# Kernel optimization log

Hardware: AMD Instinct MI355X
Metric: run time of the kernel (lower is better)

## Reference

```python
import jax, jax.numpy as jnp
import numpy as np

B, L, C_IN = 8, 1024, 12
D_MODEL, D_STATE, D_CONV, D_INNER, DT_RANK = 128, 16, 4, 256, 8
H, HD = 4, 32
LSTM_H, FC_H, NCLS = 128, 128, 5


def setup_inputs():
    ks = jax.random.split(jax.random.key(0), 16)

    def rn(k, shape, s=0.02):
        return jax.random.normal(k, shape, dtype=jnp.float32) * s

    return {
        "x": jax.random.normal(ks[0], (B, L, C_IN), dtype=jnp.float32),
        "mamba_proj_w": rn(ks[1], (C_IN, D_MODEL)),
        "mamba_proj_b": jnp.zeros((D_MODEL,), jnp.float32),
        "in_proj_w": rn(ks[2], (D_MODEL, 2 * D_INNER)),
        "conv_w": rn(ks[3], (D_INNER, D_CONV), 0.2),
        "conv_b": jnp.zeros((D_INNER,), jnp.float32),
        "x_proj_w": rn(ks[4], (D_INNER, DT_RANK + 2 * D_STATE)),
        "dt_proj_w": rn(ks[5], (DT_RANK, D_INNER), 0.1),
        "dt_proj_b": jnp.full((D_INNER,), -4.6, jnp.float32),
        "A_log": jnp.log(jnp.broadcast_to(jnp.arange(1, D_STATE + 1, dtype=jnp.float32), (D_INNER, D_STATE))),
        "Dp": jnp.ones((D_INNER,), jnp.float32),
        "out_proj_w": rn(ks[6], (D_INNER, D_MODEL)),
        "lstm_w_ih": rn(ks[7], (C_IN, 4 * LSTM_H), 0.05),
        "lstm_w_hh": rn(ks[8], (LSTM_H, 4 * LSTM_H), 0.05),
        "lstm_b": jnp.zeros((4 * LSTM_H,), jnp.float32),
        "ca_w": rn(ks[9], (2, 4, D_MODEL, D_MODEL)),
        "ca_b": jnp.zeros((2, 4, D_MODEL), jnp.float32),
        "ln_g": jnp.ones((2, D_MODEL), jnp.float32),
        "ln_b": jnp.zeros((2, D_MODEL), jnp.float32),
        "fc1_w": rn(ks[10], (2 * D_MODEL, FC_H)),
        "fc1_b": jnp.zeros((FC_H,), jnp.float32),
        "fc2_w": rn(ks[11], (FC_H, NCLS)),
        "fc2_b": jnp.zeros((NCLS,), jnp.float32),
    }


def _ln(x, g, b):
    m = jnp.mean(x, -1, keepdims=True)
    v = jnp.var(x, -1, keepdims=True)
    return (x - m) * jax.lax.rsqrt(v + 1e-5) * g + b


def _cross_attn(q_in, kv_in, w, b):
    # w: (4, d_model, d_model) q,k,v,out; b: (4, d_model)
    bsz, lq, lk = q_in.shape[0], q_in.shape[1], kv_in.shape[1]
    Q = (q_in @ w[0] + b[0]).reshape(bsz, lq, H, HD).transpose(0, 2, 1, 3)
    K = (kv_in @ w[1] + b[1]).reshape(bsz, lk, H, HD).transpose(0, 2, 1, 3)
    V = (kv_in @ w[2] + b[2]).reshape(bsz, lk, H, HD).transpose(0, 2, 1, 3)
    s = jnp.einsum('bhqd,bhkd->bhqk', Q, K) / float(np.sqrt(HD))
    a = jax.nn.softmax(s, axis=-1)
    o = jnp.einsum('bhqk,bhkd->bhqd', a, V).transpose(0, 2, 1, 3).reshape(bsz, lq, H * HD)
    return o @ w[3] + b[3]


def _mamba(u, in_proj_w, conv_w, conv_b, x_proj_w, dt_proj_w, dt_proj_b, A_log, Dp, out_proj_w):
    # u: (B, L, d_model) -> (B, L, d_model); standard Mamba selective-scan block
    xz = u @ in_proj_w  # (B, L, 2*d_inner)
    xm, z = jnp.split(xz, 2, axis=-1)
    # causal depthwise conv1d (kernel d_conv, left-padded)
    xp = jnp.pad(xm, ((0, 0), (D_CONV - 1, 0), (0, 0)))
    xc = sum(xp[:, k:k + xm.shape[1], :] * conv_w[:, k] for k in range(D_CONV)) + conv_b
    xc = jax.nn.silu(xc)  # (B, L, d_inner)
    dbl = xc @ x_proj_w
    dt = dbl[..., :DT_RANK]
    Bm = dbl[..., DT_RANK:DT_RANK + D_STATE]
    Cm = dbl[..., DT_RANK + D_STATE:]
    delta = jax.nn.softplus(dt @ dt_proj_w + dt_proj_b)  # (B, L, d_inner)
    A = -jnp.exp(A_log)  # (d_inner, d_state)
    dA = jnp.exp(delta[..., None] * A)                          # (B, L, d_inner, d_state)
    dBu = delta[..., None] * Bm[:, :, None, :] * xc[..., None]  # (B, L, d_inner, d_state)

    def step(h, inp):
        dA_t, dBu_t = inp
        h = dA_t * h + dBu_t
        return h, h

    h0 = jnp.zeros((xc.shape[0], D_INNER, D_STATE), xc.dtype)
    _, hs = jax.lax.scan(step, h0, (dA.swapaxes(0, 1), dBu.swapaxes(0, 1)))  # hs: (L, B, d_inner, d_state)
    y = jnp.einsum('lbds,bls->bld', hs, Cm) + Dp * xc
    y = y * jax.nn.silu(z)
    return y @ out_proj_w


def _forward(x, mamba_proj_w, mamba_proj_b, in_proj_w, conv_w, conv_b, x_proj_w, dt_proj_w, dt_proj_b, A_log, Dp, out_proj_w, lstm_w_ih, lstm_w_hh, lstm_b, ca_w, ca_b, ln_g, ln_b, fc1_w, fc1_b, fc2_w, fc2_b):
    H_M = _mamba(x @ mamba_proj_w + mamba_proj_b, in_proj_w, conv_w, conv_b, x_proj_w, dt_proj_w, dt_proj_b, A_log, Dp, out_proj_w)

    def lstm_step(carry, x_t):
        h, c = carry
        g = x_t @ lstm_w_ih + h @ lstm_w_hh + lstm_b
        i, f, gg, o = jnp.split(g, 4, axis=-1)  # torch gate order i,f,g,o
        c = jax.nn.sigmoid(f) * c + jax.nn.sigmoid(i) * jnp.tanh(gg)
        h = jax.nn.sigmoid(o) * jnp.tanh(c)
        return (h, c), h

    h0 = jnp.zeros((x.shape[0], LSTM_H), x.dtype)
    _, hs = jax.lax.scan(lstm_step, (h0, h0), x.swapaxes(0, 1))
    H_L = hs.swapaxes(0, 1)  # lstm_proj is Identity (lstm_hidden == d_model)

    H_Lu = _ln(H_L + _cross_attn(H_L, H_M, ca_w[0], ca_b[0]), ln_g[0], ln_b[0])
    H_Mu = _ln(H_M + _cross_attn(H_M, H_L, ca_w[1], ca_b[1]), ln_g[1], ln_b[1])
    fused = jnp.concatenate([H_Mu.mean(1), H_Lu.mean(1)], axis=1)  # (B, 2*d_model)
    return jax.nn.relu(fused @ fc1_w + fc1_b) @ fc2_w + fc2_b


def reference(x, mamba_proj_w, mamba_proj_b, in_proj_w, conv_w, conv_b, x_proj_w, dt_proj_w, dt_proj_b, A_log, Dp, out_proj_w, lstm_w_ih, lstm_w_hh, lstm_b, ca_w, ca_b, ln_g, ln_b, fc1_w, fc1_b, fc2_w, fc2_b):
    return _forward(x, mamba_proj_w, mamba_proj_b, in_proj_w, conv_w, conv_b, x_proj_w, dt_proj_w, dt_proj_b, A_log, Dp, out_proj_w, lstm_w_ih, lstm_w_hh, lstm_b, ca_w, ca_b, ln_g, ln_b, fc1_w, fc1_b, fc2_w, fc2_b)
```

## Files before the change

### kernel.cpp

```cpp
#include <hip/hip_runtime.h>
#include <hip/hip_bf16.h>
#include <math.h>

#define B_     8
#define L_     1024
#define BL_    8192
#define C_IN_  12
#define DM_    128
#define DS_    16
#define DC_    4
#define DI_    256
#define DTR_   8
#define NH_    4
#define HD_    32
#define LH_    128
#define FCH_   128
#define NCLS_  5

#define OFF_U      0u
#define OFF_XC     1048576u
#define OFF_DBL    3145728u
#define OFF_DELTA  3670016u
#define OFF_YG     5767168u
#define OFF_XZ     7864320u
#define OFF_XG     12058624u
#define OFF_HM     12058624u
#define OFF_HL     0u
#define OFF_PL     1048576u
#define OFF_PM     4194304u
#define OFF_AO0    7340032u
#define OFF_AO1    8388608u
#define OFF_T0     9437184u
#define OFF_T1     10485760u
#define OFF_WPK    14155776u
#define OFF_HLU    14286848u
#define OFF_HMU    15335424u
#define OFF_POOL   16384000u

static __device__ __forceinline__ float fexpf_(float x){ return __builtin_amdgcn_exp2f(x*1.44269504089f); }
static __device__ __forceinline__ float fsig(float x){ return __builtin_amdgcn_rcpf(1.f + fexpf_(-x)); }
static __device__ __forceinline__ float ftanh(float x){ return 1.f - 2.f*__builtin_amdgcn_rcpf(1.f + fexpf_(2.f*x)); }
static __device__ __forceinline__ float siluf(float x){ return x*fsig(x); }
static __device__ __forceinline__ float softplusf(float x){
  return (x > 0.f) ? x + log1pf(expf(-x)) : log1pf(expf(x));
}
static __device__ __forceinline__ float qbcast_xor1(float x){
  return __int_as_float(__builtin_amdgcn_mov_dpp(__float_as_int(x), 0xB1, 0xF, 0xF, true));
}
static __device__ __forceinline__ float qbcast_xor2(float x){
  return __int_as_float(__builtin_amdgcn_mov_dpp(__float_as_int(x), 0x4E, 0xF, 0xF, true));
}

__global__ __launch_bounds__(256) void gemm_kernel(
    const float* __restrict__ A, int lda,
    const float* __restrict__ W,
    const float* __restrict__ bias,
    float* __restrict__ C,
    int M, int N, int K, int act)
{
  __shared__ float As[64][17];
  __shared__ float Ws[16][65];
  const int tid = threadIdx.x;
  const int tx = tid & 15, ty = tid >> 4;
  const int m0 = blockIdx.y * 64, n0 = blockIdx.x * 64;
  float acc[4][4];
  #pragma unroll
  for (int i=0;i<4;i++)
    #pragma unroll
    for (int j=0;j<4;j++) acc[i][j]=0.f;

  for (int k0=0;k0<K;k0+=16){
    const int ar = tid >> 2, ac4 = (tid & 3) * 4;
    #pragma unroll
    for (int j=0;j<4;j++){
      int kk = k0 + ac4 + j;
      As[ar][ac4+j] = (kk < K) ? A[(size_t)(m0+ar)*lda + kk] : 0.f;
    }
    const int wc = tid & 63, wr0 = (tid >> 6) * 4;
    #pragma unroll
    for (int j=0;j<4;j++){
      int kk = k0 + wr0 + j;
      Ws[wr0+j][wc] = (kk < K && (n0+wc) < N) ? W[(size_t)kk*N + n0 + wc] : 0.f;
    }
    __syncthreads();
    #pragma unroll
    for (int kk=0;kk<16;kk++){
      float a[4], w[4];
      #pragma unroll
      for (int i=0;i<4;i++) a[i] = As[ty*4+i][kk];
      #pragma unroll
      for (int j=0;j<4;j++) w[j] = Ws[kk][tx*4+j];
      #pragma unroll
      for (int i=0;i<4;i++)
        #pragma unroll
        for (int j=0;j<4;j++)
          acc[i][j] = fmaf(a[i], w[j], acc[i][j]);
    }
    __syncthreads();
  }
  #pragma unroll
  for (int i=0;i<4;i++){
    int m = m0 + ty*4 + i;
    #pragma unroll
    for (int j=0;j<4;j++){
      int n = n0 + tx*4 + j;
      if (n < N){
        float v = acc[i][j] + (bias ? bias[n] : 0.f);
        if (act == 1) v = softplusf(v);
        C[(size_t)m*N + n] = v;
      }
    }
  }
}

__global__ __launch_bounds__(256,2) void gemm128_kernel(
    const float* __restrict__ A, int lda,
    const float* __restrict__ W,
    const float* __restrict__ bias,
    float* __restrict__ C,
    int M, int N, int K, int act)
{
  __shared__ float As[8][132];
  __shared__ float Ws[8][132];
  const int tid = threadIdx.x;
  const int tx = tid & 15, ty = tid >> 4;
  const int m0 = blockIdx.y * 128, n0 = blockIdx.x * 128;
  const int ar = tid >> 1, akq = (tid & 1) * 4;
  const int wkr = tid >> 5, wnc = (tid & 31) * 4;
  float acc[8][8];
  #pragma unroll
  for (int i=0;i<8;i++)
    #pragma unroll
    for (int j=0;j<8;j++) acc[i][j]=0.f;

  for (int k0=0;k0<K;k0+=8){
    float4 av = *(const float4*)&A[(size_t)(m0+ar)*lda + k0 + akq];
    float4 wv = *(const float4*)&W[(size_t)(k0+wkr)*N + n0 + wnc];
    __syncthreads();
    As[akq+0][ar]=av.x; As[akq+1][ar]=av.y; As[akq+2][ar]=av.z; As[akq+3][ar]=av.w;
    *(float4*)&Ws[wkr][wnc] = wv;
    __syncthreads();
    #pragma unroll
    for (int kk=0;kk<8;kk++){
      float4 a0 = *(const float4*)&As[kk][ty*8];
      float4 a1 = *(const float4*)&As[kk][ty*8+4];
      float4 w0 = *(const float4*)&Ws[kk][tx*8];
      float4 w1 = *(const float4*)&Ws[kk][tx*8+4];
      float a[8] = {a0.x,a0.y,a0.z,a0.w,a1.x,a1.y,a1.z,a1.w};
      float w[8] = {w0.x,w0.y,w0.z,w0.w,w1.x,w1.y,w1.z,w1.w};
      #pragma unroll
      for (int i=0;i<8;i++)
        #pragma unroll
        for (int j=0;j<8;j++)
          acc[i][j] = fmaf(a[i], w[j], acc[i][j]);
    }
  }
  #pragma unroll
  for (int i=0;i<8;i++){
    int m = m0 + ty*8 + i;
    #pragma unroll
    for (int j=0;j<8;j++){
      int n = n0 + tx*8 + j;
      float v = acc[i][j] + (bias ? bias[n] : 0.f);
      if (act == 1) v = softplusf(v);
      C[(size_t)m*N + n] = v;
    }
  }
}

__global__ __launch_bounds__(256) void conv_silu_kernel(
    const float* __restrict__ xz, const float* __restrict__ conv_w,
    const float* __restrict__ conv_b, float* __restrict__ xc)
{
  int idx = blockIdx.x * 256 + threadIdx.x;
  if (idx >= BL_*DI_) return;
  int d = idx & (DI_-1);
  int bl = idx >> 8;
  int l = bl & (L_-1), b = bl >> 10;
  float acc = conv_b[d];
  #pragma unroll
  for (int k=0;k<DC_;k++){
    int lk = l - (DC_-1) + k;
    if (lk >= 0)
      acc = fmaf(xz[((size_t)((b<<10)|lk))*512 + d], conv_w[d*DC_+k], acc);
  }
  xc[idx] = siluf(acc);
}

__global__ __launch_bounds__(512,2) void scan_lstm_kernel(
    const float* __restrict__ delta, const float* __restrict__ dbl,
    const float* __restrict__ xc, const float* __restrict__ xz,
    const float* __restrict__ A_log, const float* __restrict__ Dp,
    float* __restrict__ yg,
    const float* __restrict__ xg, const float* __restrict__ w_hh,
    float* __restrict__ HL)
{
  __shared__ float sd[32][32], sx[32][32], sz[32][32];
  __shared__ float sB[32][17], sC[32][17];
  __shared__ float lh[2][128];
  const int tid = threadIdx.x;

  if (blockIdx.x < 64){
    const int b = blockIdx.x >> 3;
    const int d0 = (blockIdx.x & 7) * 32;
    const int dl = tid >> 4, s = tid & 15;
    const float A = -expf(A_log[(d0+dl)*DS_ + s]);
    const float Dv = Dp[d0+dl];
    float h = 0.f;
    const size_t base = (size_t)b * L_;
    for (int t0=0; t0<L_; t0+=32){
      __syncthreads();
      #pragma unroll
      for (int i0=0;i0<2;i0++){
        int i = tid + i0*512;
        int tl = i >> 5, e = i & 31;
        size_t r = base + t0 + tl;
        sd[tl][e] = delta[r*256 + d0 + e];
        sx[tl][e] = xc[r*256 + d0 + e];
        sz[tl][e] = xz[r*512 + 256 + d0 + e];
      }
      {
        int tl = tid >> 4, e = tid & 15;
        size_t r = base + t0 + tl;
        sB[tl][e] = dbl[r*40 + DTR_ + e];
        sC[tl][e] = dbl[r*40 + DTR_ + DS_ + e];
      }
      __syncthreads();
      for (int j=0;j<32;j++){
        float dlt = sd[j][dl], xcv = sx[j][dl];
        float Bv = sB[j][s], Cv = sC[j][s];
        h = fmaf(fexpf_(dlt*A), h, (dlt*Bv)*xcv);
        float pr = h * Cv;
        pr += qbcast_xor1(pr);
        pr += qbcast_xor2(pr);
        pr += __shfl_xor(pr, 4);
        pr += __shfl_xor(pr, 8);
        if (s == 0){
          float y = pr + Dv * xcv;
          yg[(base + t0 + j)*256 + d0 + dl] = y * siluf(sz[j][dl]);
        }
      }
    }
  } else {
    const int b = blockIdx.x - 64;
    const int g = tid >> 2, p = tid & 3;
    float wi[32], wf[32], wg_[32], wo[32];
    #pragma unroll
    for (int jj=0;jj<8;jj++){
      const int j = (jj + 2*p) & 7;
      const float* wr = w_hh + (size_t)(32*p + 4*j)*512 + g;
      #pragma unroll
      for (int c=0;c<4;c++){
        wi [4*jj+c] = wr[(size_t)c*512];
        wf [4*jj+c] = wr[(size_t)c*512 + 128];
        wg_[4*jj+c] = wr[(size_t)c*512 + 256];
        wo [4*jj+c] = wr[(size_t)c*512 + 384];
      }
    }
    #pragma unroll
    for (int i=0;i<32;i++)
      asm volatile("" : "+v"(wi[i]), "+v"(wf[i]), "+v"(wg_[i]), "+v"(wo[i]));
    if (tid < 128) lh[0][tid] = 0.f;
    float creg = 0.f;
    const float* xgb = xg + (size_t)b * L_ * 512;
    float* HLb = HL + (size_t)b * L_ * 128;
    float xv0 = xgb[g], xv1 = xgb[128+g], xv2 = xgb[256+g], xv3 = xgb[384+g];
    __syncthreads();
    int cur = 0;
    for (int t=0;t<L_;t++){
      const float* hb = lh[cur] + 32*p;
      float a_i=0,a_f=0,a_g=0,a_o=0;
      #pragma unroll
      for (int jj=0;jj<8;jj++){
        const int j = (jj + 2*p) & 7;
        float4 hv = *(const float4*)(hb + 4*j);
        a_i = fmaf(hv.x, wi [4*jj+0], a_i);
        a_f = fmaf(hv.x, wf [4*jj+0], a_f);
        a_g = fmaf(hv.x, wg_[4*jj+0], a_g);
        a_o = fmaf(hv.x, wo [4*jj+0], a_o);
        a_i = fmaf(hv.y, wi [4*jj+1], a_i);
        a_f = fmaf(hv.y, wf [4*jj+1], a_f);
        a_g = fmaf(hv.y, wg_[4*jj+1], a_g);
        a_o = fmaf(hv.y, wo [4*jj+1], a_o);
        a_i = fmaf(hv.z, wi [4*jj+2], a_i);
        a_f = fmaf(hv.z, wf [4*jj+2], a_f);
        a_g = fmaf(hv.z, wg_[4*jj+2], a_g);
        a_o = fmaf(hv.z, wo [4*jj+2], a_o);
        a_i = fmaf(hv.w, wi [4*jj+3], a_i);
        a_f = fmaf(hv.w, wf [4*jj+3], a_f);
        a_g = fmaf(hv.w, wg_[4*jj+3], a_g);
        a_o = fmaf(hv.w, wo [4*jj+3], a_o);
      }
      float xn0=0.f,xn1=0.f,xn2=0.f,xn3=0.f;
      if (t+1 < L_){
        const float* xr = xgb + (size_t)(t+1)*512;
        xn0 = xr[g]; xn1 = xr[128+g]; xn2 = xr[256+g]; xn3 = xr[384+g];
      }
      a_i += qbcast_xor1(a_i); a_i += qbcast_xor2(a_i);
      a_f += qbcast_xor1(a_f); a_f += qbcast_xor2(a_f);
      a_g += qbcast_xor1(a_g); a_g += qbcast_xor2(a_g);
      a_o += qbcast_xor1(a_o); a_o += qbcast_xor2(a_o);
      float c = fsig(a_f + xv1)*creg + fsig(a_i + xv0)*ftanh(a_g + xv2);
      float hval = fsig(a_o + xv3)*ftanh(c);
      creg = c;
      if (p == 0){
        lh[cur^1][g] = hval;
        HLb[t*128 + g] = hval;
      }
      __syncthreads();
      cur ^= 1;
      xv0=xn0; xv1=xn1; xv2=xn2; xv3=xn3;
    }
  }
}

__global__ __launch_bounds__(256) void pack_kernel(
    const float* __restrict__ ca_w, const float* __restrict__ ca_b,
    float* __restrict__ wpk)
{
  int idx = blockIdx.x * 256 + threadIdx.x;
  if (idx >= 49152) return;
  int in = idx / 384, c = idx % 384;
  int seg = c >> 7, o = c & 127;
  int dL = (seg==0)?0:1;
  int iL = (seg==0)?0:((seg==1)?1:2);
  int dM = (seg==2)?1:0;
  int iM = (seg==0)?1:((seg==1)?2:0);
  wpk[idx]         = ca_w[(((size_t)(dL*4+iL))*128 + in)*128 + o];
  wpk[49152 + idx] = ca_w[(((size_t)(dM*4+iM))*128 + in)*128 + o];
  if (in == 0){
    wpk[98304 + c] = ca_b[(dL*4+iL)*128 + o];
    wpk[98688 + c] = ca_b[(dM*4+iM)*128 + o];
  }
}

__global__ __launch_bounds__(512,2) void attn_kernel(
    const float* __restrict__ PL, const float* __restrict__ PM,
    float* __restrict__ AO)
{
  __shared__ float Kt[2][32][32];
  __shared__ float Vt[2][32][32];
  __shared__ float po[256][33];
  __shared__ float pml[256][2];
  const int tid = threadIdx.x;
  const int q = tid & 255, half = tid >> 8;
  const int dir = blockIdx.z;
  const int bh = blockIdx.y;
  const int b = bh >> 2, hh = bh & 3;
  const int qg = blockIdx.x * 256 + q;
  const float* Qb; const float* Kb; const float* Vb;
  if (dir == 0){ Qb = PL;       Kb = PM;       Vb = PM + 128; }
  else         { Qb = PM + 256; Kb = PL + 128; Vb = PL + 256; }
  const size_t rowb = (size_t)b * L_;
  float qv[32];
  {
    const float4* qp = (const float4*)(Qb + (rowb + qg)*384 + hh*32);
    #pragma unroll
    for (int j=0;j<8;j++){
      float4 v = qp[j];
      qv[4*j]=v.x; qv[4*j+1]=v.y; qv[4*j+2]=v.z; qv[4*j+3]=v.w;
    }
  }
  #pragma unroll
  for (int i=0;i<32;i++) asm volatile("" : "+v"(qv[i]));
  float o[32];
  #pragma unroll
  for (int j=0;j<32;j++) o[j]=0.f;
  float m = -1e30f, l = 0.f;
  const float scale = 0.17677669529663687f;
  const int kbase = half * 512;
  for (int k0=0;k0<512;k0+=32){
    __syncthreads();
    #pragma unroll
    for (int i0=0;i0<4;i0++){
      int i = q + i0*256;
      int r = i >> 5, c = i & 31;
      Kt[half][r][c] = Kb[(rowb + kbase + k0 + r)*384 + hh*32 + c];
      Vt[half][r][c] = Vb[(rowb + kbase + k0 + r)*384 + hh*32 + c];
    }
    __syncthreads();
    for (int kk=0;kk<32;kk++){
      float d0=0.f,d1=0.f,d2=0.f,d3=0.f;
      #pragma unroll
      for (int j=0;j<32;j+=4){
        d0 = fmaf(qv[j],   Kt[half][kk][j],   d0);
        d1 = fmaf(qv[j+1], Kt[half][kk][j+1], d1);
        d2 = fmaf(qv[j+2], Kt[half][kk][j+2], d2);
        d3 = fmaf(qv[j+3], Kt[half][kk][j+3], d3);
      }
      float s4 = ((d0+d1)+(d2+d3))*scale;
      if (s4 > m + 8.f){
        float corr = fexpf_(m - s4);
        l *= corr;
        #pragma unroll
        for (int j=0;j<32;j++) o[j] *= corr;
        m = s4;
      }
      float p = fexpf_(s4 - m);
      l += p;
      #pragma unroll
      for (int j=0;j<32;j++) o[j] = fmaf(p, Vt[half][kk][j], o[j]);
    }
  }
  if (half == 1){
    pml[q][0] = m; pml[q][1] = l;
    #pragma unroll
    for (int j=0;j<32;j++) po[q][j] = o[j];
  }
  __syncthreads();
  if (half == 0){
    float m1 = pml[q][0], l1 = pml[q][1];
    float mm = fmaxf(m, m1);
    float c0 = fexpf_(m - mm), c1 = fexpf_(m1 - mm);
    float linv = 1.f / (l*c0 + l1*c1);
    float* op = AO + (size_t)dir*BL_*128 + (rowb + qg)*128 + hh*32;
    #pragma unroll
    for (int j=0;j<32;j+=4){
      float4 v;
      v.x = (o[j]*c0   + po[q][j]*c1)  *linv;
      v.y = (o[j+1]*c0 + po[q][j+1]*c1)*linv;
      v.z = (o[j+2]*c0 + po[q][j+2]*c1)*linv;
      v.w = (o[j+3]*c0 + po[q][j+3]*c1)*linv;
      *(float4*)(op + j) = v;
    }
  }
}

__global__ __launch_bounds__(64) void ln_kernel(
    const float* __restrict__ HL, const float* __restrict__ T0,
    const float* __restrict__ HM, const float* __restrict__ T1,
    const float* __restrict__ ln_g, const float* __restrict__ ln_b,
    float* __restrict__ HLu, float* __restrict__ HMu)
{
  const int row = blockIdx.x;
  const int which = blockIdx.y;
  const float* X = which ? HM : HL;
  const float* T = which ? T1 : T0;
  const float* g = ln_g + which*128;
  const float* bb = ln_b + which*128;
  float* O = which ? HMu : HLu;
  const int lane = threadIdx.x;
  float v0 = X[(size_t)row*128 + lane]      + T[(size_t)row*128 + lane];
  float v1 = X[(size_t)row*128 + 64 + lane] + T[(size_t)row*128 + 64 + lane];
  float s = v0 + v1, s2 = v0*v0 + v1*v1;
  #pragma unroll
  for (int off=1; off<64; off<<=1){ s += __shfl_xor(s,off); s2 += __shfl_xor(s2,off); }
  float mean = s * (1.f/128.f);
  float var = s2 * (1.f/128.f) - mean*mean;
  float r = rsqrtf(var + 1e-5f);
  O[(size_t)row*128 + lane]      = (v0 - mean)*r*g[lane]      + bb[lane];
  O[(size_t)row*128 + 64 + lane] = (v1 - mean)*r*g[64+lane]   + bb[64+lane];
}

__global__ __launch_bounds__(128) void pool_kernel(
    const float* __restrict__ HMu, const float* __restrict__ HLu,
    float* __restrict__ pooled)
{
  const int whichhalf = blockIdx.x;
  const int b = blockIdx.y;
  const int d = threadIdx.x;
  const float* S = whichhalf ? HLu : HMu;
  float s = 0.f;
  for (int t=0;t<L_;t++) s += S[((size_t)b*L_ + t)*128 + d];
  pooled[b*256 + whichhalf*128 + d] = s * (1.f/1024.f);
}

__global__ __launch_bounds__(128) void fc_kernel(
    const float* __restrict__ pooled,
    const float* __restrict__ fc1_w, const float* __restrict__ fc1_b,
    const float* __restrict__ fc2_w, const float* __restrict__ fc2_b,
    float* __restrict__ out)
{
  const int b = blockIdx.x;
  const int j = threadIdx.x;
  __shared__ float hid[128];
  float acc = fc1_b[j];
  for (int k=0;k<256;k++) acc = fmaf(pooled[b*256 + k], fc1_w[k*128 + j], acc);
  hid[j] = fmaxf(acc, 0.f);
  __syncthreads();
  if (j < NCLS_){
    float a = fc2_b[j];
    for (int k=0;k<128;k++) a = fmaf(hid[k], fc2_w[k*NCLS_ + j], a);
    out[b*NCLS_ + j] = a;
  }
}

extern "C" void kernel_launch(void* const* d_in, const int* in_sizes, int n_in,
                              void* d_out, int out_size, void* d_ws, size_t ws_size,
                              hipStream_t stream)
{
  const float* x            = (const float*)d_in[0];
  const float* mamba_proj_w = (const float*)d_in[1];
  const float* mamba_proj_b = (const float*)d_in[2];
  const float* in_proj_w    = (const float*)d_in[3];
  const float* conv_w       = (const float*)d_in[4];
  const float* conv_b       = (const float*)d_in[5];
  const float* x_proj_w     = (const float*)d_in[6];
  const float* dt_proj_w    = (const float*)d_in[7];
  const float* dt_proj_b    = (const float*)d_in[8];
  const float* A_log        = (const float*)d_in[9];
  const float* Dp           = (const float*)d_in[10];
  const float* out_proj_w   = (const float*)d_in[11];
  const float* lstm_w_ih    = (const float*)d_in[12];
  const float* lstm_w_hh    = (const float*)d_in[13];
  const float* lstm_b       = (const float*)d_in[14];
  const float* ca_w         = (const float*)d_in[15];
  const float* ca_b         = (const float*)d_in[16];
  const float* ln_g         = (const float*)d_in[17];
  const float* ln_b         = (const float*)d_in[18];
  const float* fc1_w        = (const float*)d_in[19];
  const float* fc1_b        = (const float*)d_in[20];
  const float* fc2_w        = (const float*)d_in[21];
  const float* fc2_b        = (const float*)d_in[22];

  float* ws     = (float*)d_ws;
  float* u      = ws + OFF_U;
  float* xc     = ws + OFF_XC;
  float* dbl    = ws + OFF_DBL;
  float* delta  = ws + OFF_DELTA;
  float* yg     = ws + OFF_YG;
  float* xz     = ws + OFF_XZ;
  float* xg     = ws + OFF_XG;
  float* HM     = ws + OFF_HM;
  float* HL     = ws + OFF_HL;
  float* wpk    = ws + OFF_WPK;
  float* PLb    = ws + OFF_PL;
  float* PMb    = ws + OFF_PM;
  float* AObase = ws + OFF_AO0;
  float* AO0    = ws + OFF_AO0;
  float* AO1    = ws + OFF_AO1;
  float* T0     = ws + OFF_T0;
  float* T1     = ws + OFF_T1;
  float* HLu    = ws + OFF_HLU;
  float* HMu    = ws + OFF_HMU;
  float* pooled = ws + OFF_POOL;

  gemm_kernel<<<dim3(2,128),256,0,stream>>>(x, 12, mamba_proj_w, mamba_proj_b, u, BL_, 128, 12, 0);
  gemm128_kernel<<<dim3(4,64),256,0,stream>>>(u, 128, in_proj_w, nullptr, xz, BL_, 512, 128, 0);
  conv_silu_kernel<<<dim3(BL_*DI_/256),256,0,stream>>>(xz, conv_w, conv_b, xc);
  gemm_kernel<<<dim3(1,128),256,0,stream>>>(xc, 256, x_proj_w, nullptr, dbl, BL_, 40, 256, 0);
  gemm128_kernel<<<dim3(2,64),256,0,stream>>>(dbl, 40, dt_proj_w, dt_proj_b, delta, BL_, 256, 8, 1);
  gemm_kernel<<<dim3(8,128),256,0,stream>>>(x, 12, lstm_w_ih, lstm_b, xg, BL_, 512, 12, 0);

  scan_lstm_kernel<<<dim3(72),512,0,stream>>>(delta, dbl, xc, xz, A_log, Dp, yg,
                                              xg, lstm_w_hh, HL);

  gemm128_kernel<<<dim3(1,64),256,0,stream>>>(yg, 256, out_proj_w, nullptr, HM, BL_, 128, 256, 0);
  pack_kernel<<<dim3(192),256,0,stream>>>(ca_w, ca_b, wpk);
  gemm128_kernel<<<dim3(3,64),256,0,stream>>>(HL, 128, wpk,         wpk + 98304, PLb, BL_, 384, 128, 0);
  gemm128_kernel<<<dim3(3,64),256,0,stream>>>(HM, 128, wpk + 49152, wpk + 98688, PMb, BL_, 384, 128, 0);
  attn_kernel<<<dim3(4,32,2),512,0,stream>>>(PLb, PMb, AObase);
  gemm128_kernel<<<dim3(1,64),256,0,stream>>>(AO0, 128, ca_w + 3*16384, ca_b + 384, T0, BL_, 128, 128, 0);
  gemm128_kernel<<<dim3(1,64),256,0,stream>>>(AO1, 128, ca_w + 7*16384, ca_b + 896, T1, BL_, 128, 128, 0);

  ln_kernel<<<dim3(8192,2),64,0,stream>>>(HL, T0, HM, T1, ln_g, ln_b, HLu, HMu);
  pool_kernel<<<dim3(2,8),128,0,stream>>>(HMu, HLu, pooled);
  fc_kernel<<<dim3(8),128,0,stream>>>(pooled, fc1_w, fc1_b, fc2_w, fc2_b, (float*)d_out);
}
```

Measured before the change: 1.416 ms.

## Repack LSTM gates with packed FMA, split attention keys across waves, remap GEMM columns

The LSTM recurrence now gives each thread two hidden units with gate-interleaved xg columns, produced by repacking lstm_w_ih and lstm_b in pack_kernel. It uses v_pk_fma_f32 and DPP reductions so each step's serial path is shorter. Attention splits the 1024 keys across 16 waves per block, reads K/V directly from global memory, uses packed FMAs, and merges partial softmax states through shared memory. The grid grows from 4 to 32 query blocks. The gemm128 column mapping is changed to reduce LDS bank conflicts, the scan inner loop is unrolled with paired LDS loads and DPP row rotates in place of shuffles, and the workspace layout is reshuffled.

```diff
diff --git a/kernel.cpp b/kernel.cpp
--- a/kernel.cpp
+++ b/kernel.cpp
@@ -20,22 +20,24 @@
 #define OFF_U      0u
 #define OFF_XC     1048576u
 #define OFF_DBL    3145728u
+#define OFF_WPK    3473408u
 #define OFF_DELTA  3670016u
 #define OFF_YG     5767168u
 #define OFF_XZ     7864320u
 #define OFF_XG     12058624u
-#define OFF_HM     12058624u
 #define OFF_HL     0u
-#define OFF_PL     1048576u
-#define OFF_PM     4194304u
-#define OFF_AO0    7340032u
-#define OFF_AO1    8388608u
-#define OFF_T0     9437184u
-#define OFF_T1     10485760u
-#define OFF_WPK    14155776u
-#define OFF_HLU    14286848u
-#define OFF_HMU    15335424u
+#define OFF_PL     4194304u
+#define OFF_PM     7340032u
+#define OFF_AO0    10485760u
+#define OFF_AO1    11534336u
+#define OFF_HM     12582912u
+#define OFF_T0     13631488u
+#define OFF_T1     14680064u
+#define OFF_HLU    1048576u
+#define OFF_HMU    2097152u
 #define OFF_POOL   16384000u
+
+typedef float v2f __attribute__((ext_vector_type(2)));
 
 static __device__ __forceinline__ float fexpf_(float x){ return __builtin_amdgcn_exp2f(x*1.44269504089f); }
 static __device__ __forceinline__ float fsig(float x){ return __builtin_amdgcn_rcpf(1.f + fexpf_(-x)); }
@@ -44,12 +46,19 @@
 static __device__ __forceinline__ float softplusf(float x){
   return (x > 0.f) ? x + log1pf(expf(-x)) : log1pf(expf(x));
 }
-static __device__ __forceinline__ float qbcast_xor1(float x){
+static __device__ __forceinline__ float qx1(float x){
   return __int_as_float(__builtin_amdgcn_mov_dpp(__float_as_int(x), 0xB1, 0xF, 0xF, true));
 }
-static __device__ __forceinline__ float qbcast_xor2(float x){
+static __device__ __forceinline__ float qx2(float x){
   return __int_as_float(__builtin_amdgcn_mov_dpp(__float_as_int(x), 0x4E, 0xF, 0xF, true));
 }
+static __device__ __forceinline__ float ror8(float x){
+  return __int_as_float(__builtin_amdgcn_mov_dpp(__float_as_int(x), 0x128, 0xF, 0xF, true));
+}
+static __device__ __forceinline__ float ror4(float x){
+  return __int_as_float(__builtin_amdgcn_mov_dpp(__float_as_int(x), 0x124, 0xF, 0xF, true));
+}
+#define PKFMA(acc, a, b) asm("v_pk_fma_f32 %0, %1, %2, %0" : "+v"(acc) : "v"(a), "v"(b))
 
 __global__ __launch_bounds__(256) void gemm_kernel(
     const float* __restrict__ A, int lda,
@@ -144,8 +153,8 @@
     for (int kk=0;kk<8;kk++){
       float4 a0 = *(const float4*)&As[kk][ty*8];
       float4 a1 = *(const float4*)&As[kk][ty*8+4];
-      float4 w0 = *(const float4*)&Ws[kk][tx*8];
-      float4 w1 = *(const float4*)&Ws[kk][tx*8+4];
+      float4 w0 = *(const float4*)&Ws[kk][tx*4];
+      float4 w1 = *(const float4*)&Ws[kk][64 + tx*4];
       float a[8] = {a0.x,a0.y,a0.z,a0.w,a1.x,a1.y,a1.z,a1.w};
       float w[8] = {w0.x,w0.y,w0.z,w0.w,w1.x,w1.y,w1.z,w1.w};
       #pragma unroll
@@ -160,7 +169,7 @@
     int m = m0 + ty*8 + i;
     #pragma unroll
     for (int j=0;j<8;j++){
-      int n = n0 + tx*8 + j;
+      int n = n0 + ((j<4) ? (tx*4 + j) : (64 + tx*4 + j - 4));
       float v = acc[i][j] + (bias ? bias[n] : 0.f);
       if (act == 1) v = softplusf(v);
       C[(size_t)m*N + n] = v;
@@ -187,135 +196,9 @@
   xc[idx] = siluf(acc);
 }
 
-__global__ __launch_bounds__(512,2) void scan_lstm_kernel(
-    const float* __restrict__ delta, const float* __restrict__ dbl,
-    const float* __restrict__ xc, const float* __restrict__ xz,
-    const float* __restrict__ A_log, const float* __restrict__ Dp,
-    float* __restrict__ yg,
-    const float* __restrict__ xg, const float* __restrict__ w_hh,
-    float* __restrict__ HL)
-{
-  __shared__ float sd[32][32], sx[32][32], sz[32][32];
-  __shared__ float sB[32][17], sC[32][17];
-  __shared__ float lh[2][128];
-  const int tid = threadIdx.x;
-
-  if (blockIdx.x < 64){
-    const int b = blockIdx.x >> 3;
-    const int d0 = (blockIdx.x & 7) * 32;
-    const int dl = tid >> 4, s = tid & 15;
-    const float A = -expf(A_log[(d0+dl)*DS_ + s]);
-    const float Dv = Dp[d0+dl];
-    float h = 0.f;
-    const size_t base = (size_t)b * L_;
-    for (int t0=0; t0<L_; t0+=32){
-      __syncthreads();
-      #pragma unroll
-      for (int i0=0;i0<2;i0++){
-        int i = tid + i0*512;
-        int tl = i >> 5, e = i & 31;
-        size_t r = base + t0 + tl;
-        sd[tl][e] = delta[r*256 + d0 + e];
-        sx[tl][e] = xc[r*256 + d0 + e];
-        sz[tl][e] = xz[r*512 + 256 + d0 + e];
-      }
-      {
-        int tl = tid >> 4, e = tid & 15;
-        size_t r = base + t0 + tl;
-        sB[tl][e] = dbl[r*40 + DTR_ + e];
-        sC[tl][e] = dbl[r*40 + DTR_ + DS_ + e];
-      }
-      __syncthreads();
-      for (int j=0;j<32;j++){
-        float dlt = sd[j][dl], xcv = sx[j][dl];
-        float Bv = sB[j][s], Cv = sC[j][s];
-        h = fmaf(fexpf_(dlt*A), h, (dlt*Bv)*xcv);
-        float pr = h * Cv;
-        pr += qbcast_xor1(pr);
-        pr += qbcast_xor2(pr);
-        pr += __shfl_xor(pr, 4);
-        pr += __shfl_xor(pr, 8);
-        if (s == 0){
-          float y = pr + Dv * xcv;
-          yg[(base + t0 + j)*256 + d0 + dl] = y * siluf(sz[j][dl]);
-        }
-      }
-    }
-  } else {
-    const int b = blockIdx.x - 64;
-    const int g = tid >> 2, p = tid & 3;
-    float wi[32], wf[32], wg_[32], wo[32];
-    #pragma unroll
-    for (int jj=0;jj<8;jj++){
-      const int j = (jj + 2*p) & 7;
-      const float* wr = w_hh + (size_t)(32*p + 4*j)*512 + g;
-      #pragma unroll
-      for (int c=0;c<4;c++){
-        wi [4*jj+c] = wr[(size_t)c*512];
-        wf [4*jj+c] = wr[(size_t)c*512 + 128];
-        wg_[4*jj+c] = wr[(size_t)c*512 + 256];
-        wo [4*jj+c] = wr[(size_t)c*512 + 384];
-      }
-    }
-    #pragma unroll
-    for (int i=0;i<32;i++)
-      asm volatile("" : "+v"(wi[i]), "+v"(wf[i]), "+v"(wg_[i]), "+v"(wo[i]));
-    if (tid < 128) lh[0][tid] = 0.f;
-    float creg = 0.f;
-    const float* xgb = xg + (size_t)b * L_ * 512;
-    float* HLb = HL + (size_t)b * L_ * 128;
-    float xv0 = xgb[g], xv1 = xgb[128+g], xv2 = xgb[256+g], xv3 = xgb[384+g];
-    __syncthreads();
-    int cur = 0;
-    for (int t=0;t<L_;t++){
-      const float* hb = lh[cur] + 32*p;
-      float a_i=0,a_f=0,a_g=0,a_o=0;
-      #pragma unroll
-      for (int jj=0;jj<8;jj++){
-        const int j = (jj + 2*p) & 7;
-        float4 hv = *(const float4*)(hb + 4*j);
-        a_i = fmaf(hv.x, wi [4*jj+0], a_i);
-        a_f = fmaf(hv.x, wf [4*jj+0], a_f);
-        a_g = fmaf(hv.x, wg_[4*jj+0], a_g);
-        a_o = fmaf(hv.x, wo [4*jj+0], a_o);
-        a_i = fmaf(hv.y, wi [4*jj+1], a_i);
-        a_f = fmaf(hv.y, wf [4*jj+1], a_f);
-        a_g = fmaf(hv.y, wg_[4*jj+1], a_g);
-        a_o = fmaf(hv.y, wo [4*jj+1], a_o);
-        a_i = fmaf(hv.z, wi [4*jj+2], a_i);
-        a_f = fmaf(hv.z, wf [4*jj+2], a_f);
-        a_g = fmaf(hv.z, wg_[4*jj+2], a_g);
-        a_o = fmaf(hv.z, wo [4*jj+2], a_o);
-        a_i = fmaf(hv.w, wi [4*jj+3], a_i);
-        a_f = fmaf(hv.w, wf [4*jj+3], a_f);
-        a_g = fmaf(hv.w, wg_[4*jj+3], a_g);
-        a_o = fmaf(hv.w, wo [4*jj+3], a_o);
-      }
-      float xn0=0.f,xn1=0.f,xn2=0.f,xn3=0.f;
-      if (t+1 < L_){
-        const float* xr = xgb + (size_t)(t+1)*512;
-        xn0 = xr[g]; xn1 = xr[128+g]; xn2 = xr[256+g]; xn3 = xr[384+g];
-      }
-      a_i += qbcast_xor1(a_i); a_i += qbcast_xor2(a_i);
-      a_f += qbcast_xor1(a_f); a_f += qbcast_xor2(a_f);
-      a_g += qbcast_xor1(a_g); a_g += qbcast_xor2(a_g);
-      a_o += qbcast_xor1(a_o); a_o += qbcast_xor2(a_o);
-      float c = fsig(a_f + xv1)*creg + fsig(a_i + xv0)*ftanh(a_g + xv2);
-      float hval = fsig(a_o + xv3)*ftanh(c);
-      creg = c;
-      if (p == 0){
-        lh[cur^1][g] = hval;
-        HLb[t*128 + g] = hval;
-      }
-      __syncthreads();
-      cur ^= 1;
-      xv0=xn0; xv1=xn1; xv2=xn2; xv3=xn3;
-    }
-  }
-}
-
 __global__ __launch_bounds__(256) void pack_kernel(
     const float* __restrict__ ca_w, const float* __restrict__ ca_b,
+    const float* __restrict__ lstm_w_ih, const float* __restrict__ lstm_b,
     float* __restrict__ wpk)
 {
   int idx = blockIdx.x * 256 + threadIdx.x;
@@ -332,98 +215,226 @@
     wpk[98304 + c] = ca_b[(dL*4+iL)*128 + o];
     wpk[98688 + c] = ca_b[(dM*4+iM)*128 + o];
   }
-}
-
-__global__ __launch_bounds__(512,2) void attn_kernel(
+  if (idx < 6144){
+    int inr = idx >> 9, cp = idx & 511;
+    int g = cp >> 2, q = cp & 3;
+    wpk[99072 + idx] = lstm_w_ih[inr*512 + q*128 + g];
+  }
+  if (idx < 512){
+    int g = idx >> 2, q = idx & 3;
+    wpk[105216 + idx] = lstm_b[q*128 + g];
+  }
+}
+
+__global__ __launch_bounds__(512) __attribute__((amdgpu_waves_per_eu(2,2)))
+void scan_lstm_kernel(
+    const float* __restrict__ delta, const float* __restrict__ dbl,
+    const float* __restrict__ xc, const float* __restrict__ xz,
+    const float* __restrict__ A_log, const float* __restrict__ Dp,
+    float* __restrict__ yg,
+    const float* __restrict__ xg, const float* __restrict__ w_hh,
+    float* __restrict__ HL)
+{
+  __shared__ v2f  sdx[32][32];
+  __shared__ v2f  sBC[32][16];
+  __shared__ float sz[32][32];
+  __shared__ __align__(16) float lh[2][128];
+  const int tid = threadIdx.x;
+
+  if (blockIdx.x < 64){
+    const int b = blockIdx.x >> 3;
+    const int d0 = (blockIdx.x & 7) * 32;
+    const int dl = tid >> 4, s = tid & 15;
+    const float A = -expf(A_log[(d0+dl)*DS_ + s]);
+    const float Dv = Dp[d0+dl];
+    float h = 0.f;
+    const size_t base = (size_t)b * L_;
+    for (int t0=0; t0<L_; t0+=32){
+      __syncthreads();
+      #pragma unroll
+      for (int i0=0;i0<2;i0++){
+        int i = tid + i0*512;
+        int tl = i >> 5, e = i & 31;
+        size_t r = base + t0 + tl;
+        v2f dx; dx.x = delta[r*256 + d0 + e]; dx.y = xc[r*256 + d0 + e];
+        sdx[tl][e] = dx;
+        sz[tl][e] = xz[r*512 + 256 + d0 + e];
+      }
+      {
+        int tl = tid >> 4, e = tid & 15;
+        size_t r = base + t0 + tl;
+        v2f bcv; bcv.x = dbl[r*40 + DTR_ + e]; bcv.y = dbl[r*40 + DTR_ + DS_ + e];
+        sBC[tl][e] = bcv;
+      }
+      __syncthreads();
+      #pragma unroll 4
+      for (int j=0;j<32;j++){
+        v2f dx = sdx[j][dl];
+        v2f bc = sBC[j][s];
+        float dlt = dx.x, xcv = dx.y;
+        h = fmaf(fexpf_(dlt*A), h, (dlt*bc.x)*xcv);
+        float pr = h * bc.y;
+        pr += qx1(pr); pr += qx2(pr); pr += ror8(pr); pr += ror4(pr);
+        if (s == 0){
+          float y = pr + Dv * xcv;
+          yg[(base + t0 + j)*256 + d0 + dl] = y * siluf(sz[j][dl]);
+        }
+      }
+    }
+  } else {
+    const int b = blockIdx.x - 64;
+    const int r  = (tid & 3) | ((tid & 8) >> 1);
+    const int g2 = ((tid & 4) >> 2) | ((tid >> 4) << 1);
+    v2f wI0[8],wI1[8],wF0[8],wF1[8],wG0[8],wG1[8],wO0[8],wO1[8];
+    #pragma unroll
+    for (int i=0;i<4;i++){
+      const int qq = (i + r) & 3;
+      #pragma unroll
+      for (int half=0; half<2; half++){
+        const int k0 = 16*r + 4*qq + 2*half;
+        const float* wb = w_hh + (size_t)k0*512 + 2*g2;
+        const int sx = 2*i + half;
+        v2f t;
+        t.x=wb[0];   t.y=wb[512]; wI0[sx]=t;
+        t.x=wb[1];   t.y=wb[513]; wI1[sx]=t;
+        t.x=wb[128]; t.y=wb[640]; wF0[sx]=t;
+        t.x=wb[129]; t.y=wb[641]; wF1[sx]=t;
+        t.x=wb[256]; t.y=wb[768]; wG0[sx]=t;
+        t.x=wb[257]; t.y=wb[769]; wG1[sx]=t;
+        t.x=wb[384]; t.y=wb[896]; wO0[sx]=t;
+        t.x=wb[385]; t.y=wb[897]; wO1[sx]=t;
+      }
+    }
+    if (tid < 128) lh[0][tid] = 0.f;
+    float creg0 = 0.f, creg1 = 0.f;
+    const float* xpb = xg + (size_t)b * L_ * 512;
+    float* HLb = HL + (size_t)b * L_ * 128;
+    float4 xa = *(const float4*)(xpb + 8*g2);
+    float4 xb = *(const float4*)(xpb + 8*g2 + 4);
+    __syncthreads();
+    int cur = 0;
+    for (int t=0;t<L_;t++){
+      const float* hb = lh[cur];
+      v2f aI0={0.f,0.f},aI1={0.f,0.f},aF0={0.f,0.f},aF1={0.f,0.f};
+      v2f aG0={0.f,0.f},aG1={0.f,0.f},aO0={0.f,0.f},aO1={0.f,0.f};
+      #pragma unroll
+      for (int i=0;i<4;i++){
+        const int qq = (i + r) & 3;
+        float4 hv = *(const float4*)(hb + 16*r + 4*qq);
+        v2f ha; ha.x=hv.x; ha.y=hv.y;
+        v2f hc; hc.x=hv.z; hc.y=hv.w;
+        PKFMA(aI0, ha, wI0[2*i]); PKFMA(aI0, hc, wI0[2*i+1]);
+        PKFMA(aI1, ha, wI1[2*i]); PKFMA(aI1, hc, wI1[2*i+1]);
+        PKFMA(aF0, ha, wF0[2*i]); PKFMA(aF0, hc, wF0[2*i+1]);
+        PKFMA(aF1, ha, wF1[2*i]); PKFMA(aF1, hc, wF1[2*i+1]);
+        PKFMA(aG0, ha, wG0[2*i]); PKFMA(aG0, hc, wG0[2*i+1]);
+        PKFMA(aG1, ha, wG1[2*i]); PKFMA(aG1, hc, wG1[2*i+1]);
+        PKFMA(aO0, ha, wO0[2*i]); PKFMA(aO0, hc, wO0[2*i+1]);
+        PKFMA(aO1, ha, wO1[2*i]); PKFMA(aO1, hc, wO1[2*i+1]);
+      }
+      float4 xna = xa, xnb = xb;
+      if (t+1 < L_){
+        xna = *(const float4*)(xpb + (size_t)(t+1)*512 + 8*g2);
+        xnb = *(const float4*)(xpb + (size_t)(t+1)*512 + 8*g2 + 4);
+      }
+      float aI0s=aI0.x+aI0.y, aI1s=aI1.x+aI1.y, aF0s=aF0.x+aF0.y, aF1s=aF1.x+aF1.y;
+      float aG0s=aG0.x+aG0.y, aG1s=aG1.x+aG1.y, aO0s=aO0.x+aO0.y, aO1s=aO1.x+aO1.y;
+      aI0s += qx1(aI0s); aI0s += qx2(aI0s); aI0s += ror8(aI0s);
+      aI1s += qx1(aI1s); aI1s += qx2(aI1s); aI1s += ror8(aI1s);
+      aF0s += qx1(aF0s); aF0s += qx2(aF0s); aF0s += ror8(aF0s);
+      aF1s += qx1(aF1s); aF1s += qx2(aF1s); aF1s += ror8(aF1s);
+      aG0s += qx1(aG0s); aG0s += qx2(aG0s); aG0s += ror8(aG0s);
+      aG1s += qx1(aG1s); aG1s += qx2(aG1s); aG1s += ror8(aG1s);
+      aO0s += qx1(aO0s); aO0s += qx2(aO0s); aO0s += ror8(aO0s);
+      aO1s += qx1(aO1s); aO1s += qx2(aO1s); aO1s += ror8(aO1s);
+      float c0 = fsig(aF0s + xa.y)*creg0 + fsig(aI0s + xa.x)*ftanh(aG0s + xa.z);
+      float h0 = fsig(aO0s + xa.w)*ftanh(c0);
+      float c1 = fsig(aF1s + xb.y)*creg1 + fsig(aI1s + xb.x)*ftanh(aG1s + xb.z);
+      float h1 = fsig(aO1s + xb.w)*ftanh(c1);
+      creg0 = c0; creg1 = c1;
+      if (r == 0){
+        v2f hw; hw.x=h0; hw.y=h1;
+        *(v2f*)(lh[cur^1] + 2*g2) = hw;
+        *(v2f*)(HLb + (size_t)t*128 + 2*g2) = hw;
+      }
+      __syncthreads();
+      cur ^= 1;
+      xa = xna; xb = xnb;
+    }
+  }
+}
+
+__global__ __launch_bounds__(512) __attribute__((amdgpu_waves_per_eu(2)))
+void attn_kernel(
     const float* __restrict__ PL, const float* __restrict__ PM,
     float* __restrict__ AO)
 {
-  __shared__ float Kt[2][32][32];
-  __shared__ float Vt[2][32][32];
-  __shared__ float po[256][33];
-  __shared__ float pml[256][2];
+  __shared__ v2f  po2[16][32][17];
+  __shared__ float sml[16][32][2];
   const int tid = threadIdx.x;
-  const int q = tid & 255, half = tid >> 8;
+  const int sp = tid >> 5, row = tid & 31;
   const int dir = blockIdx.z;
   const int bh = blockIdx.y;
   const int b = bh >> 2, hh = bh & 3;
-  const int qg = blockIdx.x * 256 + q;
+  const int qg = blockIdx.x * 32 + row;
   const float* Qb; const float* Kb; const float* Vb;
   if (dir == 0){ Qb = PL;       Kb = PM;       Vb = PM + 128; }
   else         { Qb = PM + 256; Kb = PL + 128; Vb = PL + 256; }
   const size_t rowb = (size_t)b * L_;
-  float qv[32];
+  v2f q2[16];
   {
-    const float4* qp = (const float4*)(Qb + (rowb + qg)*384 + hh*32);
-    #pragma unroll
-    for (int j=0;j<8;j++){
-      float4 v = qp[j];
-      qv[4*j]=v.x; qv[4*j+1]=v.y; qv[4*j+2]=v.z; qv[4*j+3]=v.w;
-    }
-  }
-  #pragma unroll
-  for (int i=0;i<32;i++) asm volatile("" : "+v"(qv[i]));
-  float o[32];
-  #pragma unroll
-  for (int j=0;j<32;j++) o[j]=0.f;
+    const v2f* qp = (const v2f*)(Qb + (rowb + qg)*384 + hh*32);
+    #pragma unroll
+    for (int j=0;j<16;j++) q2[j] = qp[j];
+  }
+  v2f o2[16];
+  #pragma unroll
+  for (int j=0;j<16;j++){ o2[j].x = 0.f; o2[j].y = 0.f; }
   float m = -1e30f, l = 0.f;
   const float scale = 0.17677669529663687f;
-  const int kbase = half * 512;
-  for (int k0=0;k0<512;k0+=32){
-    __syncthreads();
-    #pragma unroll
-    for (int i0=0;i0<4;i0++){
-      int i = q + i0*256;
-      int r = i >> 5, c = i & 31;
-      Kt[half][r][c] = Kb[(rowb + kbase + k0 + r)*384 + hh*32 + c];
-      Vt[half][r][c] = Vb[(rowb + kbase + k0 + r)*384 + hh*32 + c];
-    }
-    __syncthreads();
-    for (int kk=0;kk<32;kk++){
-      float d0=0.f,d1=0.f,d2=0.f,d3=0.f;
-      #pragma unroll
-      for (int j=0;j<32;j+=4){
-        d0 = fmaf(qv[j],   Kt[half][kk][j],   d0);
-        d1 = fmaf(qv[j+1], Kt[half][kk][j+1], d1);
-        d2 = fmaf(qv[j+2], Kt[half][kk][j+2], d2);
-        d3 = fmaf(qv[j+3], Kt[half][kk][j+3], d3);
-      }
-      float s4 = ((d0+d1)+(d2+d3))*scale;
-      if (s4 > m + 8.f){
-        float corr = fexpf_(m - s4);
-        l *= corr;
-        #pragma unroll
-        for (int j=0;j<32;j++) o[j] *= corr;
-        m = s4;
-      }
-      float p = fexpf_(s4 - m);
-      l += p;
-      #pragma unroll
-      for (int j=0;j<32;j++) o[j] = fmaf(p, Vt[half][kk][j], o[j]);
-    }
-  }
-  if (half == 1){
-    pml[q][0] = m; pml[q][1] = l;
-    #pragma unroll
-    for (int j=0;j<32;j++) po[q][j] = o[j];
-  }
+  for (int kk=0;kk<64;kk++){
+    const int k = sp*64 + kk;
+    const v2f* kr = (const v2f*)(Kb + (rowb + k)*384 + hh*32);
+    const v2f* vr = (const v2f*)(Vb + (rowb + k)*384 + hh*32);
+    v2f d2a={0.f,0.f}, d2b={0.f,0.f};
+    #pragma unroll
+    for (int j=0;j<16;j+=2){ PKFMA(d2a, q2[j], kr[j]); PKFMA(d2b, q2[j+1], kr[j+1]); }
+    float s4 = ((d2a.x+d2b.x)+(d2a.y+d2b.y))*scale;
+    if (s4 > m + 8.f){
+      float corr = fexpf_(m - s4);
+      l *= corr;
+      #pragma unroll
+      for (int j=0;j<16;j++){ o2[j].x *= corr; o2[j].y *= corr; }
+      m = s4;
+    }
+    float p = fexpf_(s4 - m);
+    l += p;
+    v2f p2; p2.x=p; p2.y=p;
+    #pragma unroll
+    for (int j=0;j<16;j++) PKFMA(o2[j], p2, vr[j]);
+  }
+  #pragma unroll
+  for (int j=0;j<16;j++) po2[sp][row][j] = o2[j];
+  sml[sp][row][0] = m; sml[sp][row][1] = l;
   __syncthreads();
-  if (half == 0){
-    float m1 = pml[q][0], l1 = pml[q][1];
-    float mm = fmaxf(m, m1);
-    float c0 = fexpf_(m - mm), c1 = fexpf_(m1 - mm);
-    float linv = 1.f / (l*c0 + l1*c1);
-    float* op = AO + (size_t)dir*BL_*128 + (rowb + qg)*128 + hh*32;
-    #pragma unroll
-    for (int j=0;j<32;j+=4){
-      float4 v;
-      v.x = (o[j]*c0   + po[q][j]*c1)  *linv;
-      v.y = (o[j+1]*c0 + po[q][j+1]*c1)*linv;
-      v.z = (o[j+2]*c0 + po[q][j+2]*c1)*linv;
-      v.w = (o[j+3]*c0 + po[q][j+3]*c1)*linv;
-      *(float4*)(op + j) = v;
-    }
-  }
+  const int mr = tid >> 4, dp = tid & 15;
+  float M = -1e30f;
+  #pragma unroll
+  for (int s2=0;s2<16;s2++) M = fmaxf(M, sml[s2][mr][0]);
+  float Lt = 0.f;
+  v2f acc; acc.x=0.f; acc.y=0.f;
+  #pragma unroll
+  for (int s2=0;s2<16;s2++){
+    float w = fexpf_(sml[s2][mr][0] - M);
+    Lt = fmaf(sml[s2][mr][1], w, Lt);
+    v2f t = po2[s2][mr][dp];
+    v2f w2; w2.x=w; w2.y=w;
+    PKFMA(acc, t, w2);
+  }
+  float inv = __builtin_amdgcn_rcpf(Lt);
+  float* op = AO + (size_t)dir*BL_*128 + (rowb + blockIdx.x*32 + mr)*128 + hh*32;
+  v2f outv; outv.x = acc.x*inv; outv.y = acc.y*inv;
+  *(v2f*)(op + 2*dp) = outv;
 }
 
 __global__ __launch_bounds__(64) void ln_kernel(
@@ -535,21 +546,22 @@
   float* HMu    = ws + OFF_HMU;
   float* pooled = ws + OFF_POOL;
 
+  pack_kernel<<<dim3(192),256,0,stream>>>(ca_w, ca_b, lstm_w_ih, lstm_b, wpk);
+
   gemm_kernel<<<dim3(2,128),256,0,stream>>>(x, 12, mamba_proj_w, mamba_proj_b, u, BL_, 128, 12, 0);
   gemm128_kernel<<<dim3(4,64),256,0,stream>>>(u, 128, in_proj_w, nullptr, xz, BL_, 512, 128, 0);
   conv_silu_kernel<<<dim3(BL_*DI_/256),256,0,stream>>>(xz, conv_w, conv_b, xc);
   gemm_kernel<<<dim3(1,128),256,0,stream>>>(xc, 256, x_proj_w, nullptr, dbl, BL_, 40, 256, 0);
   gemm128_kernel<<<dim3(2,64),256,0,stream>>>(dbl, 40, dt_proj_w, dt_proj_b, delta, BL_, 256, 8, 1);
-  gemm_kernel<<<dim3(8,128),256,0,stream>>>(x, 12, lstm_w_ih, lstm_b, xg, BL_, 512, 12, 0);
+  gemm_kernel<<<dim3(8,128),256,0,stream>>>(x, 12, wpk + 99072, wpk + 105216, xg, BL_, 512, 12, 0);
 
   scan_lstm_kernel<<<dim3(72),512,0,stream>>>(delta, dbl, xc, xz, A_log, Dp, yg,
                                               xg, lstm_w_hh, HL);
 
   gemm128_kernel<<<dim3(1,64),256,0,stream>>>(yg, 256, out_proj_w, nullptr, HM, BL_, 128, 256, 0);
-  pack_kernel<<<dim3(192),256,0,stream>>>(ca_w, ca_b, wpk);
   gemm128_kernel<<<dim3(3,64),256,0,stream>>>(HL, 128, wpk,         wpk + 98304, PLb, BL_, 384, 128, 0);
   gemm128_kernel<<<dim3(3,64),256,0,stream>>>(HM, 128, wpk + 49152, wpk + 98688, PMb, BL_, 384, 128, 0);
-  attn_kernel<<<dim3(4,32,2),512,0,stream>>>(PLb, PMb, AObase);
+  attn_kernel<<<dim3(32,32,2),512,0,stream>>>(PLb, PMb, AObase);
   gemm128_kernel<<<dim3(1,64),256,0,stream>>>(AO0, 128, ca_w + 3*16384, ca_b + 384, T0, BL_, 128, 128, 0);
   gemm128_kernel<<<dim3(1,64),256,0,stream>>>(AO1, 128, ca_w + 7*16384, ca_b + 896, T1, BL_, 128, 128, 0);
 
```

Result: slower. 1.804 ms (+27.4%).
